# Performance work log

Measured on AMD Instinct MI355X. Metric: run time of the kernel, lower is better.

## Reference

```python
import jax, jax.numpy as jnp
import numpy as np

# Scene / model dims (match init_kwargs)
H, W, T = 128, 128, 8
N = 1024  # number of 3D (x,y,t) Gaussians, layer 0

CHOL_BOUND_3D = jnp.array([0.5, 0.0, 0.5, 0.5, 0.0, 0.5], dtype=jnp.float32)


def setup_inputs() -> dict:
    key = jax.random.key(0)
    k1, k2, k3 = jax.random.split(key, 3)
    xyz = jax.random.normal(k1, (N, 3), dtype=jnp.float32)          # raw (pre-tanh) positions
    cholesky = jax.random.uniform(k2, (N, 6), dtype=jnp.float32)    # raw cholesky params
    cholesky = cholesky.at[:, 5].add(float(T))                      # _init_layer0: data[:,5] += T
    features = jax.random.uniform(k3, (N, 3), dtype=jnp.float32)    # rgb features
    opacity = jnp.ones((N, 1), dtype=jnp.float32)                   # layer-0 opacity buffer (ones)
    background = jnp.ones((3,), dtype=jnp.float32)                  # unused by the sum-rasterizer
    return {"xyz": xyz, "cholesky": cholesky, "features": features,
            "opacity": opacity, "background": background}


def _render(xyz, cholesky, features, opacity):
    # --- project_gaussians_video ---
    # positions: tanh -> ndc (-1,1) -> pixel/frame coords (ndc2pix: 0.5*((v+1)*S - 1))
    sizes = jnp.array([W, H, T], dtype=jnp.float32)
    means = 0.5 * ((jnp.tanh(xyz) + 1.0) * sizes - 1.0)             # (N,3) in (x,y,t)
    c = cholesky + CHOL_BOUND_3D                                     # get_cholesky_elements
    # lower-triangular L, column-major packing: [L00,L10,L20,L11,L21,L22]
    L = jnp.zeros((N, 3, 3), dtype=c.dtype)
    L = L.at[:, 0, 0].set(c[:, 0]).at[:, 1, 0].set(c[:, 1]).at[:, 2, 0].set(c[:, 2])
    L = L.at[:, 1, 1].set(c[:, 3]).at[:, 2, 1].set(c[:, 4]).at[:, 2, 2].set(c[:, 5])
    cov = jnp.einsum('nij,nkj->nik', L, L)                           # Sigma = L L^T
    conic = jnp.linalg.inv(cov)                                      # (N,3,3), symmetric

    # --- rasterize_gaussians_sum_video (dense reference, no tile culling) ---
    # sigma(p) = 0.5 p^T Q p - p^T Q m + 0.5 m^T Q m, expressed as a [P,10] x [10,N] matmul
    qm = jnp.einsum('nij,nj->ni', conic, means)                      # (N,3)
    const = 0.5 * jnp.einsum('ni,ni->n', means, qm)                  # (N,)
    G = jnp.stack([0.5 * conic[:, 0, 0], 0.5 * conic[:, 1, 1], 0.5 * conic[:, 2, 2],
                   conic[:, 0, 1], conic[:, 0, 2], conic[:, 1, 2],
                   -qm[:, 0], -qm[:, 1], -qm[:, 2], const], axis=1)  # (N,10)

    ts = jnp.arange(T, dtype=jnp.float32)
    ys = jnp.arange(H, dtype=jnp.float32)
    xs = jnp.arange(W, dtype=jnp.float32)
    pt, py, px = jnp.meshgrid(ts, ys, xs, indexing='ij')             # (T,H,W) — t-major pixel order
    px, py, pt = px.ravel(), py.ravel(), pt.ravel()                  # (P,), P = T*H*W
    F = jnp.stack([px * px, py * py, pt * pt, px * py, px * pt, py * pt,
                   px, py, pt, jnp.ones_like(px)], axis=1)           # (P,10)

    sigma = F @ G.T                                                  # (P,N) — memory-bound hot loop
    wgt = jnp.exp(-sigma) * opacity[:, 0][None, :]                   # alpha per pixel/gaussian
    img = wgt @ features                                             # (P,3) alpha-weighted sum blend
    img = jnp.clip(img, 0.0, 1.0)
    # view(-1,T,H,W,3).permute(0,4,2,3,1) -> (1,3,H,W,T)
    return jnp.transpose(img.reshape(1, T, H, W, 3), (0, 4, 2, 3, 1))


def reference(xyz, cholesky, features, opacity, background):
    return _render(xyz, cholesky, features, opacity)
```

## Files before the change

kernel.cpp:

```cpp
#include <hip/hip_runtime.h>
#include <math.h>

#define HH 128
#define WW 128
#define TT 8
#define NG 1024
#define PP (HH * WW * TT)
#define NS 8
#define GS 128

__device__ __forceinline__ float fast_tanh(float x) {
    float e = __builtin_amdgcn_exp2f(x * 2.885390081777926814f);
    return 1.f - 2.f * __builtin_amdgcn_rcpf(e + 1.f);
}

__global__ __launch_bounds__(1024, 8) void gv_fused(
    const float* __restrict__ xyz,
    const float* __restrict__ chol,
    const float* __restrict__ feat,
    const float* __restrict__ opac,
    float* __restrict__ out)
{
    __shared__ __align__(16) float recs[NS][GS * 8];
    __shared__ int sidx[NS][GS];
    __shared__ int cnt_lds[16];
    __shared__ __align__(16) float4 pbuf[7][2][WW];

    const int tid = threadIdx.x;
    const int lane = tid & 63;
    const int wv = tid >> 6;
    const int s = wv >> 1;
    const int sub = wv & 1;
    const int r0 = blockIdx.x * 2;
    const float y0f = (float)(r0 & 127);
    const float tf  = (float)(r0 >> 7);
    const float kneg = -1.44269504088896340736f;

    {
        const int n = s * GS + sub * 64 + lane;
        float vy = xyz[n * 3 + 1];
        float c1 = chol[n * 6 + 1];
        float c3 = chol[n * 6 + 3] + 0.5f;
        float my = fmaf(fast_tanh(vy), 64.f, 63.5f);
        float syy = fmaf(c1, c1, c3 * c3);
        float d0 = my - y0f;
        float d1 = d0 - 1.f;
        float dmin = fminf(fabsf(d0), fabsf(d1));
        bool keep = dmin * dmin < 32.f * syy;

        unsigned long long mask = __ballot(keep);
        if (keep) {
            int pos = __builtin_amdgcn_mbcnt_hi(
                          (unsigned)(mask >> 32),
                          __builtin_amdgcn_mbcnt_lo((unsigned)mask, 0));
            sidx[s][sub * 64 + pos] = n;
        }
        if (lane == 0) cnt_lds[wv] = (int)__popcll(mask);
    }
    __syncthreads();

    {
        const int sb = tid >> 7;
        const int tq = tid & 127;
        const int cA = cnt_lds[2 * sb];
        const int Sb = cA + cnt_lds[2 * sb + 1];
        if (tq < Sb) {
            const int n = (tq < cA) ? sidx[sb][tq] : sidx[sb][64 + tq - cA];

            float vx = xyz[n * 3 + 0], vy = xyz[n * 3 + 1], vt = xyz[n * 3 + 2];
            float mx = 0.5f * ((fast_tanh(vx) + 1.f) * (float)WW - 1.f);
            float my = 0.5f * ((fast_tanh(vy) + 1.f) * (float)HH - 1.f);
            float mt = 0.5f * ((fast_tanh(vt) + 1.f) * (float)TT - 1.f);

            float c0 = chol[n * 6 + 0] + 0.5f;
            float c1 = chol[n * 6 + 1];
            float c2 = chol[n * 6 + 2] + 0.5f;
            float c3 = chol[n * 6 + 3] + 0.5f;
            float c4 = chol[n * 6 + 4];
            float c5 = chol[n * 6 + 5] + 0.5f;

            float a  = c0 * c0;
            float b  = c0 * c1;
            float cc = c0 * c2;
            float d  = c1 * c1 + c3 * c3;
            float e  = c1 * c2 + c3 * c4;
            float f  = c2 * c2 + c4 * c4 + c5 * c5;

            float A00 = d * f - e * e;
            float A01 = cc * e - b * f;
            float A02 = b * e - cc * d;
            float A11 = a * f - cc * cc;
            float A12 = b * cc - a * e;
            float A22 = a * d - b * b;
            float det = a * A00 + b * A01 + cc * A02;
            float rdet = 1.f / det;
            float Q00 = A00 * rdet, Q01 = A01 * rdet, Q02 = A02 * rdet;
            float Q11 = A11 * rdet, Q12 = A12 * rdet, Q22 = A22 * rdet;

            float qmx = Q00 * mx + Q01 * my + Q02 * mt;
            float qmy = Q01 * mx + Q11 * my + Q12 * mt;
            float qmt = Q02 * mx + Q12 * my + Q22 * mt;
            float cst = 0.5f * (mx * qmx + my * qmy + mt * qmt);

            float G0 = 0.5f * Q00, G1 = 0.5f * Q11, G2 = 0.5f * Q22;
            float G3 = Q01, G4 = Q02, G5 = Q12;
            float G6 = -qmx, G7 = -qmy, G8 = -qmt, G9 = cst;

            float u  = fmaf(G4, tf, G6);
            float v  = fmaf(G5, tf, G7);
            float w0 = fmaf(fmaf(G2, tf, G8), tf, G9);
            float B0 = fmaf(G3, y0f, u);
            float C0 = fmaf(fmaf(G1, y0f, v), y0f, w0);
            float y1f = y0f + 1.f;
            float B1 = fmaf(G3, y1f, u);
            float C1 = fmaf(fmaf(G1, y1f, v), y1f, w0);

            float op = opac[n];
            float4* l4 = (float4*)recs[sb];
            l4[tq * 2 + 0] = (float4){kneg * G0, op * feat[n * 3 + 0],
                                      op * feat[n * 3 + 1], op * feat[n * 3 + 2]};
            l4[tq * 2 + 1] = (float4){kneg * B0, kneg * C0, kneg * B1, kneg * C1};
        }
    }
    __syncthreads();

    const int S = cnt_lds[2 * s] + cnt_lds[2 * s + 1];
    const float x1 = (float)lane;
    const float x2 = x1 + 64.f;
    float a0 = 0.f, a1 = 0.f, a2 = 0.f;
    float b0 = 0.f, b1 = 0.f, b2 = 0.f;
    const float4* lds4 = (const float4*)recs[s];
    const float* recf = recs[s];

#pragma unroll 4
    for (int m = 0; m < S; ++m) {
        float4 af = lds4[m * 2];
        float2 bc = *(const float2*)&recf[m * 8 + 4 + 2 * sub];
        float s1 = fmaf(fmaf(af.x, x1, bc.x), x1, bc.y);
        float s2 = fmaf(fmaf(af.x, x2, bc.x), x2, bc.y);
        float w1 = __builtin_amdgcn_exp2f(s1);
        float w2 = __builtin_amdgcn_exp2f(s2);
        a0 = fmaf(w1, af.y, a0);
        a1 = fmaf(w1, af.z, a1);
        a2 = fmaf(w1, af.w, a2);
        b0 = fmaf(w2, af.y, b0);
        b1 = fmaf(w2, af.z, b1);
        b2 = fmaf(w2, af.w, b2);
    }

    if (s != 0) {
        pbuf[s - 1][sub][lane]      = (float4){a0, a1, a2, 0.f};
        pbuf[s - 1][sub][lane + 64] = (float4){b0, b1, b2, 0.f};
    }
    __syncthreads();

    if (s == 0) {
#pragma unroll
        for (int k = 0; k < 7; ++k) {
            float4 p = pbuf[k][sub][lane];
            float4 q = pbuf[k][sub][lane + 64];
            a0 += p.x; a1 += p.y; a2 += p.z;
            b0 += q.x; b1 += q.y; b2 += q.z;
        }

        a0 = fminf(fmaxf(a0, 0.f), 1.f);
        a1 = fminf(fmaxf(a1, 0.f), 1.f);
        a2 = fminf(fmaxf(a2, 0.f), 1.f);
        b0 = fminf(fmaxf(b0, 0.f), 1.f);
        b1 = fminf(fmaxf(b1, 0.f), 1.f);
        b2 = fminf(fmaxf(b2, 0.f), 1.f);

        const int r = r0 + sub;
        const int y = r & 127, t = r >> 7;
        const int base_o = (y * WW + lane) * TT + t;
        out[base_o] = a0;
        out[base_o + 64 * TT] = b0;
        out[base_o + PP] = a1;
        out[base_o + PP + 64 * TT] = b1;
        out[base_o + 2 * PP] = a2;
        out[base_o + 2 * PP + 64 * TT] = b2;
    }
}

extern "C" void kernel_launch(void* const* d_in, const int* in_sizes, int n_in,
                              void* d_out, int out_size, void* d_ws, size_t ws_size,
                              hipStream_t stream) {
    const float* xyz  = (const float*)d_in[0];
    const float* chol = (const float*)d_in[1];
    const float* feat = (const float*)d_in[2];
    const float* opac = (const float*)d_in[3];
    float* out = (float*)d_out;

    const int blocks = (TT * HH) / 2;
    gv_fused<<<blocks, 1024, 0, stream>>>(xyz, chol, feat, opac, out);
}
```

Baseline: 14.10 us.

## Process one row per block with per-wave culling to drop intra-block syncs

Each block now handles a single image row using 8 waves, with 1024 blocks instead of 512. Each wave culls and prepares its own 128-Gaussian slice into private LDS, so two block-wide barriers are removed and the cull test is tighter for a single row. The trade-off is that Gaussian setup math and culling are redone twice as often across blocks, and the wave-local setup loop can leave lanes idle when few Gaussians survive.

```diff
diff --git a/kernel.cpp b/kernel.cpp
--- a/kernel.cpp
+++ b/kernel.cpp
@@ -6,136 +6,122 @@
 #define TT 8
 #define NG 1024
 #define PP (HH * WW * TT)
-#define NS 8
-#define GS 128
+#define NSP 8
+#define GSP 128
 
 __device__ __forceinline__ float fast_tanh(float x) {
     float e = __builtin_amdgcn_exp2f(x * 2.885390081777926814f);
     return 1.f - 2.f * __builtin_amdgcn_rcpf(e + 1.f);
 }
 
-__global__ __launch_bounds__(1024, 8) void gv_fused(
+__global__ __launch_bounds__(512, 8) void gv_fused(
     const float* __restrict__ xyz,
     const float* __restrict__ chol,
     const float* __restrict__ feat,
     const float* __restrict__ opac,
     float* __restrict__ out)
 {
-    __shared__ __align__(16) float recs[NS][GS * 8];
-    __shared__ int sidx[NS][GS];
-    __shared__ int cnt_lds[16];
-    __shared__ __align__(16) float4 pbuf[7][2][WW];
+    __shared__ __align__(16) float recs[NSP][GSP * 8];
+    __shared__ int sidx[NSP][GSP];
+    __shared__ __align__(16) float4 pbuf[NSP - 1][2 * 64];
 
     const int tid = threadIdx.x;
     const int lane = tid & 63;
-    const int wv = tid >> 6;
-    const int s = wv >> 1;
-    const int sub = wv & 1;
-    const int r0 = blockIdx.x * 2;
-    const float y0f = (float)(r0 & 127);
-    const float tf  = (float)(r0 >> 7);
+    const int w = tid >> 6;
+    const int r = blockIdx.x;
+    const float yf = (float)(r & 127);
+    const float tf = (float)(r >> 7);
     const float kneg = -1.44269504088896340736f;
 
-    {
-        const int n = s * GS + sub * 64 + lane;
+    int cnt = 0;
+#pragma unroll
+    for (int it = 0; it < 2; ++it) {
+        const int n = w * GSP + it * 64 + lane;
         float vy = xyz[n * 3 + 1];
         float c1 = chol[n * 6 + 1];
         float c3 = chol[n * 6 + 3] + 0.5f;
         float my = fmaf(fast_tanh(vy), 64.f, 63.5f);
         float syy = fmaf(c1, c1, c3 * c3);
-        float d0 = my - y0f;
-        float d1 = d0 - 1.f;
-        float dmin = fminf(fabsf(d0), fabsf(d1));
-        bool keep = dmin * dmin < 32.f * syy;
+        float dy = my - yf;
+        bool keep = dy * dy < 32.f * syy;
 
         unsigned long long mask = __ballot(keep);
         if (keep) {
             int pos = __builtin_amdgcn_mbcnt_hi(
                           (unsigned)(mask >> 32),
                           __builtin_amdgcn_mbcnt_lo((unsigned)mask, 0));
-            sidx[s][sub * 64 + pos] = n;
+            sidx[w][cnt + pos] = n;
         }
-        if (lane == 0) cnt_lds[wv] = (int)__popcll(mask);
+        cnt += (int)__popcll(mask);
     }
-    __syncthreads();
+    const int S = cnt;
 
-    {
-        const int sb = tid >> 7;
-        const int tq = tid & 127;
-        const int cA = cnt_lds[2 * sb];
-        const int Sb = cA + cnt_lds[2 * sb + 1];
-        if (tq < Sb) {
-            const int n = (tq < cA) ? sidx[sb][tq] : sidx[sb][64 + tq - cA];
+    for (int j = lane; j < S; j += 64) {
+        const int n = sidx[w][j];
 
-            float vx = xyz[n * 3 + 0], vy = xyz[n * 3 + 1], vt = xyz[n * 3 + 2];
-            float mx = 0.5f * ((fast_tanh(vx) + 1.f) * (float)WW - 1.f);
-            float my = 0.5f * ((fast_tanh(vy) + 1.f) * (float)HH - 1.f);
-            float mt = 0.5f * ((fast_tanh(vt) + 1.f) * (float)TT - 1.f);
+        float vx = xyz[n * 3 + 0], vy = xyz[n * 3 + 1], vt = xyz[n * 3 + 2];
+        float mx = 0.5f * ((fast_tanh(vx) + 1.f) * (float)WW - 1.f);
+        float my = 0.5f * ((fast_tanh(vy) + 1.f) * (float)HH - 1.f);
+        float mt = 0.5f * ((fast_tanh(vt) + 1.f) * (float)TT - 1.f);
 
-            float c0 = chol[n * 6 + 0] + 0.5f;
-            float c1 = chol[n * 6 + 1];
-            float c2 = chol[n * 6 + 2] + 0.5f;
-            float c3 = chol[n * 6 + 3] + 0.5f;
-            float c4 = chol[n * 6 + 4];
-            float c5 = chol[n * 6 + 5] + 0.5f;
+        float c0 = chol[n * 6 + 0] + 0.5f;
+        float c1 = chol[n * 6 + 1];
+        float c2 = chol[n * 6 + 2] + 0.5f;
+        float c3 = chol[n * 6 + 3] + 0.5f;
+        float c4 = chol[n * 6 + 4];
+        float c5 = chol[n * 6 + 5] + 0.5f;
 
-            float a  = c0 * c0;
-            float b  = c0 * c1;
-            float cc = c0 * c2;
-            float d  = c1 * c1 + c3 * c3;
-            float e  = c1 * c2 + c3 * c4;
-            float f  = c2 * c2 + c4 * c4 + c5 * c5;
+        float a  = c0 * c0;
+        float b  = c0 * c1;
+        float cc = c0 * c2;
+        float d  = c1 * c1 + c3 * c3;
+        float e  = c1 * c2 + c3 * c4;
+        float f  = c2 * c2 + c4 * c4 + c5 * c5;
 
-            float A00 = d * f - e * e;
-            float A01 = cc * e - b * f;
-            float A02 = b * e - cc * d;
-            float A11 = a * f - cc * cc;
-            float A12 = b * cc - a * e;
-            float A22 = a * d - b * b;
-            float det = a * A00 + b * A01 + cc * A02;
-            float rdet = 1.f / det;
-            float Q00 = A00 * rdet, Q01 = A01 * rdet, Q02 = A02 * rdet;
-            float Q11 = A11 * rdet, Q12 = A12 * rdet, Q22 = A22 * rdet;
+        float A00 = d * f - e * e;
+        float A01 = cc * e - b * f;
+        float A02 = b * e - cc * d;
+        float A11 = a * f - cc * cc;
+        float A12 = b * cc - a * e;
+        float A22 = a * d - b * b;
+        float det = a * A00 + b * A01 + cc * A02;
+        float rdet = 1.f / det;
+        float Q00 = A00 * rdet, Q01 = A01 * rdet, Q02 = A02 * rdet;
+        float Q11 = A11 * rdet, Q12 = A12 * rdet, Q22 = A22 * rdet;
 
-            float qmx = Q00 * mx + Q01 * my + Q02 * mt;
-            float qmy = Q01 * mx + Q11 * my + Q12 * mt;
-            float qmt = Q02 * mx + Q12 * my + Q22 * mt;
-            float cst = 0.5f * (mx * qmx + my * qmy + mt * qmt);
+        float qmx = Q00 * mx + Q01 * my + Q02 * mt;
+        float qmy = Q01 * mx + Q11 * my + Q12 * mt;
+        float qmt = Q02 * mx + Q12 * my + Q22 * mt;
+        float cst = 0.5f * (mx * qmx + my * qmy + mt * qmt);
 
-            float G0 = 0.5f * Q00, G1 = 0.5f * Q11, G2 = 0.5f * Q22;
-            float G3 = Q01, G4 = Q02, G5 = Q12;
-            float G6 = -qmx, G7 = -qmy, G8 = -qmt, G9 = cst;
+        float G0 = 0.5f * Q00, G1 = 0.5f * Q11, G2 = 0.5f * Q22;
+        float G3 = Q01, G4 = Q02, G5 = Q12;
+        float G6 = -qmx, G7 = -qmy, G8 = -qmt, G9 = cst;
 
-            float u  = fmaf(G4, tf, G6);
-            float v  = fmaf(G5, tf, G7);
-            float w0 = fmaf(fmaf(G2, tf, G8), tf, G9);
-            float B0 = fmaf(G3, y0f, u);
-            float C0 = fmaf(fmaf(G1, y0f, v), y0f, w0);
-            float y1f = y0f + 1.f;
-            float B1 = fmaf(G3, y1f, u);
-            float C1 = fmaf(fmaf(G1, y1f, v), y1f, w0);
+        float u  = fmaf(G4, tf, G6);
+        float v  = fmaf(G5, tf, G7);
+        float w0 = fmaf(fmaf(G2, tf, G8), tf, G9);
+        float B  = fmaf(G3, yf, u);
+        float C  = fmaf(fmaf(G1, yf, v), yf, w0);
 
-            float op = opac[n];
-            float4* l4 = (float4*)recs[sb];
-            l4[tq * 2 + 0] = (float4){kneg * G0, op * feat[n * 3 + 0],
-                                      op * feat[n * 3 + 1], op * feat[n * 3 + 2]};
-            l4[tq * 2 + 1] = (float4){kneg * B0, kneg * C0, kneg * B1, kneg * C1};
-        }
+        float op = opac[n];
+        float4* l4 = (float4*)recs[w];
+        l4[j * 2 + 0] = (float4){kneg * G0, op * feat[n * 3 + 0],
+                                 op * feat[n * 3 + 1], op * feat[n * 3 + 2]};
+        l4[j * 2 + 1] = (float4){kneg * B, kneg * C, 0.f, 0.f};
     }
-    __syncthreads();
 
-    const int S = cnt_lds[2 * s] + cnt_lds[2 * s + 1];
     const float x1 = (float)lane;
     const float x2 = x1 + 64.f;
     float a0 = 0.f, a1 = 0.f, a2 = 0.f;
     float b0 = 0.f, b1 = 0.f, b2 = 0.f;
-    const float4* lds4 = (const float4*)recs[s];
-    const float* recf = recs[s];
+    const float4* lds4 = (const float4*)recs[w];
+    const float* recf = recs[w];
 
 #pragma unroll 4
     for (int m = 0; m < S; ++m) {
         float4 af = lds4[m * 2];
-        float2 bc = *(const float2*)&recf[m * 8 + 4 + 2 * sub];
+        float2 bc = *(const float2*)&recf[m * 8 + 4];
         float s1 = fmaf(fmaf(af.x, x1, bc.x), x1, bc.y);
         float s2 = fmaf(fmaf(af.x, x2, bc.x), x2, bc.y);
         float w1 = __builtin_amdgcn_exp2f(s1);
@@ -148,17 +134,17 @@
         b2 = fmaf(w2, af.w, b2);
     }
 
-    if (s != 0) {
-        pbuf[s - 1][sub][lane]      = (float4){a0, a1, a2, 0.f};
-        pbuf[s - 1][sub][lane + 64] = (float4){b0, b1, b2, 0.f};
+    if (w != 0) {
+        pbuf[w - 1][lane]      = (float4){a0, a1, a2, 0.f};
+        pbuf[w - 1][lane + 64] = (float4){b0, b1, b2, 0.f};
     }
     __syncthreads();
 
-    if (s == 0) {
+    if (w == 0) {
 #pragma unroll
-        for (int k = 0; k < 7; ++k) {
-            float4 p = pbuf[k][sub][lane];
-            float4 q = pbuf[k][sub][lane + 64];
+        for (int k = 0; k < NSP - 1; ++k) {
+            float4 p = pbuf[k][lane];
+            float4 q = pbuf[k][lane + 64];
             a0 += p.x; a1 += p.y; a2 += p.z;
             b0 += q.x; b1 += q.y; b2 += q.z;
         }
@@ -170,7 +156,6 @@
         b1 = fminf(fmaxf(b1, 0.f), 1.f);
         b2 = fminf(fmaxf(b2, 0.f), 1.f);
 
-        const int r = r0 + sub;
         const int y = r & 127, t = r >> 7;
         const int base_o = (y * WW + lane) * TT + t;
         out[base_o] = a0;
@@ -191,6 +176,6 @@
     const float* opac = (const float*)d_in[3];
     float* out = (float*)d_out;
 
-    const int blocks = (TT * HH) / 2;
-    gv_fused<<<blocks, 1024, 0, stream>>>(xyz, chol, feat, opac, out);
+    const int blocks = TT * HH;
+    gv_fused<<<blocks, 512, 0, stream>>>(xyz, chol, feat, opac, out);
 }
```

Result: faster. 13.54 us (-4.0%).
